# Kernel tuning notes

Hardware: AMD Instinct MI355X
Metric: run time of the kernel (lower is better)

## Reference

```python
import jax, jax.numpy as jnp
import numpy as np

B, K, H, W = 8, 1024, 24, 24
C = H * W            # in_channels = 576
NH = 6               # hardcoded num_heads
HD = C // NH         # 96


def setup_inputs() -> dict:
    key = jax.random.key(0)
    ks = jax.random.split(key, 8)
    s = 1.0 / np.sqrt(C)
    return {
        "input1": jax.random.normal(ks[0], (B, K, H, W), jnp.float32),
        "input2": jax.random.normal(ks[1], (B, K, H, W), jnp.float32),
        "Wq": jax.random.uniform(ks[2], (C, C), jnp.float32, -s, s),
        "bq": jax.random.uniform(ks[3], (C,), jnp.float32, -s, s),
        "Wk": jax.random.uniform(ks[4], (C, C), jnp.float32, -s, s),
        "bk": jax.random.uniform(ks[5], (C,), jnp.float32, -s, s),
        "Wv": jax.random.uniform(ks[6], (C, C), jnp.float32, -s, s),
        "bv": jax.random.uniform(ks[7], (C,), jnp.float32, -s, s),
    }


def reference(input1, input2, Wq, bq, Wk, bk, Wv, bv):
    b, k, h, w = input1.shape
    c = h * w
    x1 = input1.reshape(b, k, c)
    x2 = input2.reshape(b, k, c)
    # torch nn.Linear: y = x @ W^T + b
    q = x1 @ Wq.T + bq                      # [b, k, c]
    kk = x2 @ Wk.T + bk
    v = x2 @ Wv.T + bv
    # torch .view scrambles: [b, k, c] -> [b, NH, c//NH, k] (row-major reshape)
    q = q.reshape(b, NH, c // NH, k)
    kk = kk.reshape(b, NH, c // NH, k)
    v = v.reshape(b, NH, c // NH, k)
    # scores = q^T k over head-dim; NOTE: no 1/sqrt(d) scaling in original
    scores = jnp.einsum('bhdq,bhdk->bhqk', q, kk)   # [b, NH, k, k]
    weights = jax.nn.softmax(scores, axis=-1)
    # context = value @ weights^T -> [b, NH, hd, k]
    ctx = jnp.einsum('bhdk,bhqk->bhdq', v, weights)
    return ctx.reshape(b, k, h, w)
```

## Files before the change

kernel.cpp:

```cpp
#include <hip/hip_runtime.h>
#include <cmath>

#define BATCH 8
#define KDIM  1024
#define CH    576
#define NHEAD 6
#define HDIM  96

typedef _Float16 f16;
typedef f16 f16x4 __attribute__((ext_vector_type(4)));
typedef f16 f16x8 __attribute__((ext_vector_type(8)));
typedef float f32x16 __attribute__((ext_vector_type(16)));
typedef unsigned int u32;

#define PSZ  (BATCH * KDIM * CH)
#define WSZ  (CH * CH)

__device__ inline f32x16 zero16() {
    f32x16 z;
#pragma unroll
    for (int r = 0; r < 16; ++r) z[r] = 0.f;
    return z;
}

__global__ __launch_bounds__(256) void convert_kernel(
    const float* __restrict__ x1, const float* __restrict__ x2,
    const float* __restrict__ Wq, const float* __restrict__ Wk,
    const float* __restrict__ Wv,
    f16* __restrict__ x1h, f16* __restrict__ x2h, f16* __restrict__ wh)
{
    const int y = blockIdx.y;
    int idx = blockIdx.x * 256 + threadIdx.x;
    const float* src;
    f16* dst;
    if (y == 0) {
        if (idx >= PSZ / 8) return;
        src = x1; dst = x1h;
    } else if (y == 1) {
        if (idx >= PSZ / 8) return;
        src = x2; dst = x2h;
    } else {
        if (idx >= 3 * WSZ / 8) return;
        int seg = idx / (WSZ / 8);
        src = (seg == 0) ? Wq : (seg == 1) ? Wk : Wv;
        dst = wh + seg * WSZ;
        idx -= seg * (WSZ / 8);
    }
    float4 u0 = ((const float4*)src)[2 * idx];
    float4 u1 = ((const float4*)src)[2 * idx + 1];
    f16x8 hv;
    hv[0] = (f16)u0.x; hv[1] = (f16)u0.y; hv[2] = (f16)u0.z; hv[3] = (f16)u0.w;
    hv[4] = (f16)u1.x; hv[5] = (f16)u1.y; hv[6] = (f16)u1.z; hv[7] = (f16)u1.w;
    ((f16x8*)dst)[idx] = hv;
}

__global__ __launch_bounds__(256, 4) void proj_kernel(
    const f16* __restrict__ x1h, const f16* __restrict__ x2h,
    const f16* __restrict__ wh,
    const float* __restrict__ bq, const float* __restrict__ bk,
    const float* __restrict__ bv,
    f16* __restrict__ qf, f16* __restrict__ kf, f16* __restrict__ vf)
{
    const int z = blockIdx.z;
    const f16* A      = (z == 0) ? x1h : x2h;
    const f16* W      = wh + z * WSZ;
    const float* bias = (z == 0) ? bq : (z == 1) ? bk : bv;
    f16* dst          = (z == 0) ? qf : (z == 1) ? kf : vf;

    __shared__ f16 As[64 * 72];
    __shared__ f16 Ws[192 * 72];

    const int tid = threadIdx.x;
    const int lane = tid & 63, w = tid >> 6;
    const int l31 = lane & 31, half = lane >> 5;
    const int mw = 32 * (w & 1), nh = 96 * (w >> 1);
    const int nBase = blockIdx.x * 192;
    const int mBase = blockIdx.y * 64;

    int arow[2], ach[2], wrow[6], wch[6];
#pragma unroll
    for (int r = 0; r < 2; ++r) {
        int idx = r * 256 + tid;
        arow[r] = idx >> 3; ach[r] = idx & 7;
    }
#pragma unroll
    for (int r = 0; r < 6; ++r) {
        int idx = r * 256 + tid;
        wrow[r] = idx >> 3; wch[r] = idx & 7;
    }

    f16x8 aP[2], wP[6];
#pragma unroll
    for (int r = 0; r < 2; ++r)
        aP[r] = *(const f16x8*)&A[(size_t)(mBase + arow[r]) * CH + ach[r] * 8];
#pragma unroll
    for (int r = 0; r < 6; ++r)
        wP[r] = *(const f16x8*)&W[(size_t)(nBase + wrow[r]) * CH + wch[r] * 8];

    f32x16 acc[3] = {zero16(), zero16(), zero16()};

    for (int k0 = 0; k0 < CH; k0 += 64) {
        __syncthreads();
#pragma unroll
        for (int r = 0; r < 2; ++r)
            *(f16x8*)&As[arow[r] * 72 + ach[r] * 8] = aP[r];
#pragma unroll
        for (int r = 0; r < 6; ++r)
            *(f16x8*)&Ws[wrow[r] * 72 + wch[r] * 8] = wP[r];
        __syncthreads();
        if (k0 + 64 < CH) {
#pragma unroll
            for (int r = 0; r < 2; ++r)
                aP[r] = *(const f16x8*)&A[(size_t)(mBase + arow[r]) * CH + k0 + 64 + ach[r] * 8];
#pragma unroll
            for (int r = 0; r < 6; ++r)
                wP[r] = *(const f16x8*)&W[(size_t)(nBase + wrow[r]) * CH + k0 + 64 + wch[r] * 8];
        }
#pragma unroll
        for (int ks = 0; ks < 4; ++ks) {
            f16x8 a = *(const f16x8*)&As[(mw + l31) * 72 + 16 * ks + 8 * half];
#pragma unroll
            for (int nt = 0; nt < 3; ++nt) {
                f16x8 bfr = *(const f16x8*)&Ws[(nh + 32 * nt + l31) * 72 + 16 * ks + 8 * half];
                acc[nt] = __builtin_amdgcn_mfma_f32_32x32x16_f16(a, bfr, acc[nt], 0, 0, 0);
            }
        }
    }

#pragma unroll
    for (int nt = 0; nt < 3; ++nt) {
        int n = nBase + nh + 32 * nt + l31;
        float bsv = bias[n];
#pragma unroll
        for (int r = 0; r < 16; ++r) {
            int m = mBase + mw + (r & 3) + 8 * (r >> 2) + 4 * half;
            dst[(size_t)m * CH + n] = (f16)(acc[nt][r] + bsv);
        }
    }
}

__global__ __launch_bounds__(256) void transpose_qk(
    const f16* __restrict__ qf, const f16* __restrict__ kf,
    f16* __restrict__ QT, f16* __restrict__ KT)
{
    const int tt = blockIdx.x;
    const int bh = blockIdx.y;
    const f16* src = blockIdx.z ? kf : qf;
    f16* dst = blockIdx.z ? KT : QT;

    __shared__ f16 Ts[96 * 72];

    const int tid = threadIdx.x;
    const int rowbase = (bh / NHEAD) * CH + (bh % NHEAD) * HDIM;

#pragma unroll
    for (int r = 0; r < 3; ++r) {
        int idx = r * 256 + tid;
        int d = idx >> 3, g = idx & 7;
        *(f16x8*)&Ts[d * 72 + g * 8] =
            *(const f16x8*)&src[(size_t)(rowbase + d) * KDIM + tt * 64 + g * 8];
    }
    __syncthreads();
#pragma unroll
    for (int r = 0; r < 3; ++r) {
        int idx = r * 256 + tid;
        int t = idx & 63, dg = idx >> 6;
        f16x8 v;
#pragma unroll
        for (int u = 0; u < 8; ++u) v[u] = Ts[(dg * 8 + u) * 72 + t];
        *(f16x8*)&dst[((size_t)bh * KDIM + tt * 64 + t) * HDIM + dg * 8] = v;
    }
}

__global__ __launch_bounds__(256, 3) void attn_kernel(
    const f16* __restrict__ qT, const f16* __restrict__ kT,
    const f16* __restrict__ vf, float* __restrict__ out)
{
    __shared__ __align__(16) char smem[27136];
    f16* Ks = (f16*)smem;
    f16* Vs = (f16*)(smem + 13312);
    f16* Qs = Ks;

    const int bh = blockIdx.x;
    const int qt = blockIdx.y;
    const int h  = bh % NHEAD;
    const int b  = bh / NHEAD;

    const int tid = threadIdx.x;
    const int lane = tid & 63, w = tid >> 6;
    const int ih = w & 1, jg = w >> 1;
    const int l31 = lane & 31, half = lane >> 5;
    const int iw = 32 * ih;

    const f16* Qbase = qT + ((size_t)bh * KDIM + qt * 64) * HDIM;
    const f16* Kbase = kT + (size_t)bh * KDIM * HDIM;
    const f16* Vbase = vf + ((size_t)b * CH + (size_t)h * HDIM) * KDIM;

    int kt[3], kg[3], vd[3], vg[3];
#pragma unroll
    for (int r = 0; r < 3; ++r) {
        int idx = r * 256 + tid;
        kt[r] = idx / 12; kg[r] = idx % 12;
        vd[r] = idx >> 3; vg[r] = idx & 7;
    }

#pragma unroll
    for (int r = 0; r < 3; ++r)
        *(f16x8*)&Qs[kt[r] * 104 + kg[r] * 8] =
            *(const f16x8*)&Qbase[kt[r] * 96 + kg[r] * 8];
    __syncthreads();
    f16x8 qfr[6];
#pragma unroll
    for (int ks = 0; ks < 6; ++ks) {
        qfr[ks] = *(const f16x8*)&Qs[(iw + l31) * 104 + 16 * ks + 8 * half];
#pragma unroll
        for (int u = 0; u < 8; ++u)
            qfr[ks][u] = (f16)((float)qfr[ks][u] * 1.44269504f);
    }

    f16x8 kreg[3], vreg[3];
#pragma unroll
    for (int r = 0; r < 3; ++r) {
        kreg[r] = *(const f16x8*)&Kbase[(size_t)kt[r] * HDIM + kg[r] * 8];
        vreg[r] = *(const f16x8*)&Vbase[(size_t)vd[r] * KDIM + vg[r] * 8];
    }

    float l_run = 0.f;
    f32x16 Oacc[3] = {zero16(), zero16(), zero16()};

    for (int jt = 0; jt < KDIM; jt += 64) {
        __syncthreads();
#pragma unroll
        for (int r = 0; r < 3; ++r) {
            *(f16x8*)&Ks[kt[r] * 104 + kg[r] * 8] = kreg[r];
            *(f16x8*)&Vs[vd[r] * 72 + vg[r] * 8]  = vreg[r];
        }
        __syncthreads();
        if (jt + 64 < KDIM) {
#pragma unroll
            for (int r = 0; r < 3; ++r) {
                kreg[r] = *(const f16x8*)&Kbase[(size_t)(jt + 64 + kt[r]) * HDIM + kg[r] * 8];
                vreg[r] = *(const f16x8*)&Vbase[(size_t)vd[r] * KDIM + jt + 64 + vg[r] * 8];
            }
        }

        f32x16 s0 = zero16();
#pragma unroll
        for (int ks = 0; ks < 6; ++ks) {
            f16x8 ak = *(const f16x8*)&Ks[(32 * jg + l31) * 104 + 16 * ks + 8 * half];
            s0 = __builtin_amdgcn_mfma_f32_32x32x16_f16(ak, qfr[ks], s0, 0, 0, 0);
        }

        f16x4 pq[4];
#pragma unroll
        for (int r = 0; r < 16; ++r) {
            float e = __builtin_amdgcn_exp2f(s0[r] - 26.0f);
            l_run += e;
            pq[r >> 2][r & 3] = (f16)e;
        }

#pragma unroll
        for (int kc = 0; kc < 2; ++kc) {
            union { f16x4 h; u32 u[2]; } snd, rcv, keep;
            keep.h = half ? pq[2 * kc + 1] : pq[2 * kc];
            snd.h  = half ? pq[2 * kc]     : pq[2 * kc + 1];
            rcv.u[0] = __shfl_xor((int)snd.u[0], 32);
            rcv.u[1] = __shfl_xor((int)snd.u[1], 32);
            f16x8 bp;
            if (half == 0) {
#pragma unroll
                for (int v = 0; v < 4; ++v) { bp[v] = keep.h[v]; bp[4 + v] = rcv.h[v]; }
            } else {
#pragma unroll
                for (int v = 0; v < 4; ++v) { bp[v] = rcv.h[v]; bp[4 + v] = keep.h[v]; }
            }
            int jo = 32 * jg + 16 * kc + 8 * half;
#pragma unroll
            for (int t = 0; t < 3; ++t) {
                f16x8 av = *(const f16x8*)&Vs[(32 * t + l31) * 72 + jo];
                Oacc[t] = __builtin_amdgcn_mfma_f32_32x32x16_f16(av, bp, Oacc[t], 0, 0, 0);
            }
        }
    }

    l_run += __shfl_xor(l_run, 32);

    __syncthreads();
    float* Oscr = (float*)smem;
    float* lScr = (float*)(smem + 25344);
    if (jg == 1) {
        if (half == 0) lScr[iw + l31] = l_run;
        float* od = Oscr + ih * 3168;
#pragma unroll
        for (int t = 0; t < 3; ++t)
#pragma unroll
            for (int r = 0; r < 16; ++r) {
                int d = 32 * t + (r & 3) + 8 * (r >> 2) + 4 * half;
                od[d * 33 + l31] = Oacc[t][r];
            }
    }
    __syncthreads();
    if (jg == 0) {
        float linv = 1.0f / (l_run + lScr[iw + l31]);
        const float* od = Oscr + ih * 3168;
        float* obase = out + ((size_t)b * CH + (size_t)h * HDIM) * KDIM
                           + qt * 64 + iw + l31;
#pragma unroll
        for (int t = 0; t < 3; ++t)
#pragma unroll
            for (int r = 0; r < 16; ++r) {
                int d = 32 * t + (r & 3) + 8 * (r >> 2) + 4 * half;
                obase[(size_t)d * KDIM] =
                    (Oacc[t][r] + od[d * 33 + l31]) * linv;
            }
    }
}

extern "C" void kernel_launch(void* const* d_in, const int* in_sizes, int n_in,
                              void* d_out, int out_size, void* d_ws, size_t ws_size,
                              hipStream_t stream)
{
    const float* x1 = (const float*)d_in[0];
    const float* x2 = (const float*)d_in[1];
    const float* Wq = (const float*)d_in[2];
    const float* bq = (const float*)d_in[3];
    const float* Wk = (const float*)d_in[4];
    const float* bk = (const float*)d_in[5];
    const float* Wv = (const float*)d_in[6];
    const float* bv = (const float*)d_in[7];
    float* out = (float*)d_out;

    const size_t P = PSZ;
    f16* x1h = (f16*)d_ws;
    f16* x2h = x1h + P;
    f16* qf  = x2h + P;
    f16* kf  = qf + P;
    f16* vf  = kf + P;
    f16* wh  = vf + P;
    f16* QT  = x1h;
    f16* KT  = x2h;

    dim3 cgrid((P / 8 + 255) / 256, 3);
    convert_kernel<<<cgrid, 256, 0, stream>>>(x1, x2, Wq, Wk, Wv, x1h, x2h, wh);

    dim3 pgrid(CH / 192, (BATCH * KDIM) / 64, 3);
    proj_kernel<<<pgrid, 256, 0, stream>>>(x1h, x2h, wh, bq, bk, bv, qf, kf, vf);

    dim3 tgrid(KDIM / 64, BATCH * NHEAD, 2);
    transpose_qk<<<tgrid, 256, 0, stream>>>(qf, kf, QT, KT);

    dim3 agrid(BATCH * NHEAD, KDIM / 64);
    attn_kernel<<<agrid, 256, 0, stream>>>(QT, KT, vf, out);
}
```

Measured before the change: 170.9 us.

## Load K/V MFMA fragments directly from global memory instead of LDS staging

Removes the shared-memory staging of Q, K and V tiles and the per-iteration barriers. Each wave now reads its MFMA operand fragments straight from global memory, relying on L1/L2 for the reuse across waves. This removes LDS traffic and synchronization, but it duplicates global loads across the two waves sharing each K tile and the waves sharing V. It also loses the register prefetch that overlapped loads with compute, and the V reads are strided by KDIM.

```diff
diff --git a/kernel.cpp b/kernel.cpp
--- a/kernel.cpp
+++ b/kernel.cpp
@@ -176,10 +176,7 @@
     const f16* __restrict__ qT, const f16* __restrict__ kT,
     const f16* __restrict__ vf, float* __restrict__ out)
 {
-    __shared__ __align__(16) char smem[27136];
-    f16* Ks = (f16*)smem;
-    f16* Vs = (f16*)(smem + 13312);
-    f16* Qs = Ks;
+    __shared__ __align__(16) char smem[25600];
 
     const int bh = blockIdx.x;
     const int qt = blockIdx.y;
@@ -196,58 +193,27 @@
     const f16* Kbase = kT + (size_t)bh * KDIM * HDIM;
     const f16* Vbase = vf + ((size_t)b * CH + (size_t)h * HDIM) * KDIM;
 
-    int kt[3], kg[3], vd[3], vg[3];
-#pragma unroll
-    for (int r = 0; r < 3; ++r) {
-        int idx = r * 256 + tid;
-        kt[r] = idx / 12; kg[r] = idx % 12;
-        vd[r] = idx >> 3; vg[r] = idx & 7;
-    }
-
-#pragma unroll
-    for (int r = 0; r < 3; ++r)
-        *(f16x8*)&Qs[kt[r] * 104 + kg[r] * 8] =
-            *(const f16x8*)&Qbase[kt[r] * 96 + kg[r] * 8];
-    __syncthreads();
     f16x8 qfr[6];
 #pragma unroll
     for (int ks = 0; ks < 6; ++ks) {
-        qfr[ks] = *(const f16x8*)&Qs[(iw + l31) * 104 + 16 * ks + 8 * half];
+        qfr[ks] = *(const f16x8*)&Qbase[(size_t)(iw + l31) * HDIM + 16 * ks + 8 * half];
 #pragma unroll
         for (int u = 0; u < 8; ++u)
             qfr[ks][u] = (f16)((float)qfr[ks][u] * 1.44269504f);
     }
 
-    f16x8 kreg[3], vreg[3];
-#pragma unroll
-    for (int r = 0; r < 3; ++r) {
-        kreg[r] = *(const f16x8*)&Kbase[(size_t)kt[r] * HDIM + kg[r] * 8];
-        vreg[r] = *(const f16x8*)&Vbase[(size_t)vd[r] * KDIM + vg[r] * 8];
-    }
+    const f16* Kfrag = Kbase + (size_t)(32 * jg + l31) * HDIM + 8 * half;
+    const f16* Vfrag = Vbase + (size_t)l31 * KDIM;
 
     float l_run = 0.f;
     f32x16 Oacc[3] = {zero16(), zero16(), zero16()};
 
     for (int jt = 0; jt < KDIM; jt += 64) {
-        __syncthreads();
-#pragma unroll
-        for (int r = 0; r < 3; ++r) {
-            *(f16x8*)&Ks[kt[r] * 104 + kg[r] * 8] = kreg[r];
-            *(f16x8*)&Vs[vd[r] * 72 + vg[r] * 8]  = vreg[r];
-        }
-        __syncthreads();
-        if (jt + 64 < KDIM) {
-#pragma unroll
-            for (int r = 0; r < 3; ++r) {
-                kreg[r] = *(const f16x8*)&Kbase[(size_t)(jt + 64 + kt[r]) * HDIM + kg[r] * 8];
-                vreg[r] = *(const f16x8*)&Vbase[(size_t)vd[r] * KDIM + jt + 64 + vg[r] * 8];
-            }
-        }
-
         f32x16 s0 = zero16();
+        const f16* Kt = Kfrag + (size_t)jt * HDIM;
 #pragma unroll
         for (int ks = 0; ks < 6; ++ks) {
-            f16x8 ak = *(const f16x8*)&Ks[(32 * jg + l31) * 104 + 16 * ks + 8 * half];
+            f16x8 ak = *(const f16x8*)&Kt[16 * ks];
             s0 = __builtin_amdgcn_mfma_f32_32x32x16_f16(ak, qfr[ks], s0, 0, 0, 0);
         }
 
@@ -274,10 +240,10 @@
 #pragma unroll
                 for (int v = 0; v < 4; ++v) { bp[v] = rcv.h[v]; bp[4 + v] = keep.h[v]; }
             }
-            int jo = 32 * jg + 16 * kc + 8 * half;
+            const int jo = jt + 32 * jg + 16 * kc + 8 * half;
 #pragma unroll
             for (int t = 0; t < 3; ++t) {
-                f16x8 av = *(const f16x8*)&Vs[(32 * t + l31) * 72 + jo];
+                f16x8 av = *(const f16x8*)&Vfrag[(size_t)(32 * t) * KDIM + jo];
                 Oacc[t] = __builtin_amdgcn_mfma_f32_32x32x16_f16(av, bp, Oacc[t], 0, 0, 0);
             }
         }
@@ -285,7 +251,6 @@
 
     l_run += __shfl_xor(l_run, 32);
 
-    __syncthreads();
     float* Oscr = (float*)smem;
     float* lScr = (float*)(smem + 25344);
     if (jg == 1) {
```

Measured after the change: 194.4 us. 13.8% more time.
